# Kernel tuning notes

Measured on AMD Instinct MI355X. Metric: run time of the kernel, lower is better.

The kernel has to match this reference:

```python
import jax, jax.numpy as jnp
import numpy as np

ACT_BIT = 8
W_BIT = 8
EPS = 1e-8


def ste_round(x):
    # straight-through round (matches torch STE quant autograd)
    return x + jax.lax.stop_gradient(jnp.round(x) - x)


def quant_act(x):
    """Per-tensor symmetric 8-bit activation quantization (HAWQ QuantAct)."""
    n = 2 ** (ACT_BIT - 1) - 1  # 127
    x_max = jax.lax.stop_gradient(jnp.max(jnp.abs(x)))
    scale = jnp.maximum(x_max, EPS) / n
    x_int = jnp.clip(ste_round(x / scale), -n - 1, n)
    return x_int * scale, scale


def quant_linear(x_q, act_scale, weight, bias):
    """Per-channel symmetric 8-bit weight quant + integer matmul + fused dequant."""
    n = 2 ** (W_BIT - 1) - 1  # 127
    w_max = jax.lax.stop_gradient(jnp.max(jnp.abs(weight), axis=1, keepdims=True))  # [out,1]
    w_scale = jnp.maximum(w_max, EPS) / n                                            # [out,1]
    w_int = jnp.clip(ste_round(weight / w_scale), -n - 1, n)                         # [out,in]
    bias_scale = w_scale[:, 0] * act_scale                                           # [out]
    b_int = ste_round(bias / bias_scale)                                             # [out]
    x_int = x_q / act_scale                                   # integer-valued float, [..., in]
    out_int = jnp.einsum('...i,oi->...o', x_int, w_int)       # int8-domain GEMM in float
    return (out_int + b_int) * bias_scale                     # fused dequant


def setup_inputs() -> dict:
    key = jax.random.key(0)
    k1, k2, k3 = jax.random.split(key, 3)
    L, B, Q, D, O = 6, 8, 1024, 1024, 1024
    hs = jax.random.normal(k1, (L, B, Q, D), dtype=jnp.float32)
    weight = jax.random.normal(k2, (O, D), dtype=jnp.float32) * 0.02
    bias = jax.random.normal(k3, (O,), dtype=jnp.float32) * 0.02
    return {"hs": hs, "weight": weight, "bias": bias}


def reference(hs, weight, bias):
    x_q, act_scale = quant_act(hs)
    return quant_linear(x_q, act_scale, weight, bias)
```

## Files before the change

### kernel.cpp

```cpp
#include <hip/hip_runtime.h>
#include <stdint.h>

typedef int i32x4 __attribute__((ext_vector_type(4)));

#define K_DIM 1024
#define BM 256
#define BN 256
#define BKK 64
#define NKT (K_DIM / BKK)


__device__ __forceinline__ int quant1(float v, float inv) {
  float t = rintf(v * inv);
  t = fminf(fmaxf(t, -128.0f), 127.0f);
  return (int)t;
}

__device__ __forceinline__ void gld_lds16(const signed char* g, signed char* l) {
  typedef const __attribute__((address_space(1))) unsigned int* gp_t;
  typedef __attribute__((address_space(3))) unsigned int* lp_t;
  __builtin_amdgcn_global_load_lds((gp_t)(const void*)g, (lp_t)(void*)l, 16, 0, 0);
}

#define SB __builtin_amdgcn_sched_barrier(0)
#define BAR __builtin_amdgcn_s_barrier()
#define WAIT_LGKM0 asm volatile("s_waitcnt lgkmcnt(0)" ::: "memory")

__global__ void absmax_part(const float* __restrict__ x, float* __restrict__ parts,
                            long long n4) {
  long long i = (long long)blockIdx.x * blockDim.x + threadIdx.x;
  const long long stride = (long long)gridDim.x * blockDim.x;
  const float4* x4 = (const float4*)x;
  float m = 0.0f;
  for (; i < n4; i += stride) {
    float4 v = x4[i];
    m = fmaxf(m, fmaxf(fmaxf(fabsf(v.x), fabsf(v.y)), fmaxf(fabsf(v.z), fabsf(v.w))));
  }
#pragma unroll
  for (int off = 32; off > 0; off >>= 1) m = fmaxf(m, __shfl_down(m, off, 64));
  __shared__ float sm[4];
  const int lane = threadIdx.x & 63, wid = threadIdx.x >> 6;
  if (lane == 0) sm[wid] = m;
  __syncthreads();
  if (threadIdx.x == 0)
    parts[blockIdx.x] = fmaxf(fmaxf(sm[0], sm[1]), fmaxf(sm[2], sm[3]));
}

__global__ void absmax_fin(const float* __restrict__ parts, unsigned int* __restrict__ amax_u,
                           int nparts) {
  const int t = threadIdx.x;
  float m = 0.0f;
  for (int i = t; i < nparts; i += 256) m = fmaxf(m, parts[i]);
#pragma unroll
  for (int off = 32; off > 0; off >>= 1) m = fmaxf(m, __shfl_down(m, off, 64));
  __shared__ float sm[4];
  const int lane = t & 63, wid = t >> 6;
  if (lane == 0) sm[wid] = m;
  __syncthreads();
  if (t == 0)
    amax_u[0] = __float_as_uint(fmaxf(fmaxf(sm[0], sm[1]), fmaxf(sm[2], sm[3])));
}

__global__ void wquant_kernel(const float* __restrict__ w, const float* __restrict__ bias,
                              const unsigned int* __restrict__ amax_u,
                              signed char* __restrict__ wq,
                              float* __restrict__ bscale, float* __restrict__ bint) {
  const int o = blockIdx.x;
  const int t = threadIdx.x;
  float4 v = ((const float4*)(w + (size_t)o * K_DIM))[t];
  float m = fmaxf(fmaxf(fabsf(v.x), fabsf(v.y)), fmaxf(fabsf(v.z), fabsf(v.w)));
#pragma unroll
  for (int off = 32; off > 0; off >>= 1) m = fmaxf(m, __shfl_down(m, off, 64));
  __shared__ float sm[4];
  __shared__ float s_scale;
  const int lane = t & 63, wid = t >> 6;
  if (lane == 0) sm[wid] = m;
  __syncthreads();
  if (t == 0) {
    float wm = fmaxf(fmaxf(sm[0], sm[1]), fmaxf(sm[2], sm[3]));
    float wsc = fmaxf(wm, 1e-8f) / 127.0f;
    float asc = fmaxf(__uint_as_float(*amax_u), 1e-8f) / 127.0f;
    float bsc = wsc * asc;
    bscale[o] = bsc;
    bint[o] = rintf(bias[o] / bsc);
    s_scale = wsc;
  }
  __syncthreads();
  const float inv = 1.0f / s_scale;
  int q0 = quant1(v.x, inv), q1 = quant1(v.y, inv), q2 = quant1(v.z, inv), q3 = quant1(v.w, inv);
  unsigned int p = (unsigned)(q0 & 255) | ((unsigned)(q1 & 255) << 8) |
                   ((unsigned)(q2 & 255) << 16) | ((unsigned)(q3 & 255) << 24);
  const int F = o >> 4, T = t >> 4;
  const int l = (((t >> 2) & 3) << 4) | (o & 15);
  const int j = (t << 2) & 15;
  *(unsigned int*)(wq + (((size_t)F << 14) + (T << 10) + (l << 4) + j)) = p;
}

__global__ void aquant_kernel(const float* __restrict__ x, const unsigned int* __restrict__ amax_u,
                              uint4* __restrict__ q16, int nchunk) {
  const float asc = fmaxf(__uint_as_float(*amax_u), 1e-8f) / 127.0f;
  const float inv = 1.0f / asc;
  int c = blockIdx.x * blockDim.x + threadIdx.x;
  const int stride = gridDim.x * blockDim.x;
  for (; c < nchunk; c += stride) {
    const int l = c & 63, T = (c >> 6) & 15, F = c >> 10;
    const size_t src = (((size_t)(F << 4) + (l & 15)) << 10) + (T << 6) + ((l >> 4) << 4);
    const float4* s4 = (const float4*)(x + src);
    unsigned int r[4];
#pragma unroll
    for (int q = 0; q < 4; q++) {
      float4 v = s4[q];
      int q0 = quant1(v.x, inv), q1 = quant1(v.y, inv), q2 = quant1(v.z, inv), q3 = quant1(v.w, inv);
      r[q] = (unsigned)(q0 & 255) | ((unsigned)(q1 & 255) << 8) |
             ((unsigned)(q2 & 255) << 16) | ((unsigned)(q3 & 255) << 24);
    }
    q16[c] = make_uint4(r[0], r[1], r[2], r[3]);
  }
}

__global__ __launch_bounds__(512, 2) void gemm_kernel(
    const signed char* __restrict__ A, const signed char* __restrict__ W,
    const float* __restrict__ bscale, const float* __restrict__ bint,
    float* __restrict__ out, int M, int N, int K) {
  extern __shared__ __align__(16) signed char smem[];
  signed char* Abase = smem;

  const int nwg = gridDim.x;
  const int orig = blockIdx.x;
  const int wgid = (orig & 7) * (nwg >> 3) + (orig >> 3);
  const int nbn = N / BN;
  const int bm = wgid / nbn;
  const int bn = wgid % nbn;
  const int m0 = bm * BM, n0 = bn * BN;

  const int tid = threadIdx.x;
  const int lane = tid & 63;
  const int wid = tid >> 6;
  const int wr = wid >> 1 >> 1;
  const int wc = wid & 3;

  const signed char* gaf = A + (((size_t)(m0 >> 4) + wid) << 14) + (lane << 4);
  const size_t fs8 = (size_t)8 << 14;
  const signed char* gbf = W + (((size_t)(n0 >> 4) + wc * 4) << 14) + (lane << 4);

  i32x4 acc[8][4];
#pragma unroll
  for (int i = 0; i < 8; i++)
#pragma unroll
    for (int j = 0; j < 4; j++) acc[i][j] = (i32x4){0, 0, 0, 0};

  i32x4 af[8];
  i32x4 bfA[4], bfB[4];

#define LOADB(L, tt)                                                           \
  do {                                                                         \
    L[0] = *(const i32x4*)(gbf + ((size_t)0 << 14) + ((tt) << 10));            \
    L[1] = *(const i32x4*)(gbf + ((size_t)1 << 14) + ((tt) << 10));            \
    L[2] = *(const i32x4*)(gbf + ((size_t)2 << 14) + ((tt) << 10));            \
    L[3] = *(const i32x4*)(gbf + ((size_t)3 << 14) + ((tt) << 10));            \
  } while (0)

#define ISSUEA(tt)                                                             \
  do {                                                                         \
    gld_lds16(gaf + ((size_t)(tt) << 10),                                      \
              Abase + ((((tt) & 3) * 16 + wid) << 10));                        \
    gld_lds16(gaf + fs8 + ((size_t)(tt) << 10),                                \
              Abase + ((((tt) & 3) * 16 + wid + 8) << 10));                    \
  } while (0)

#define RD_A(t, i_)                                                            \
  af[i_] = *(const i32x4*)(Abase + ((((t) & 3) * 16 + wr * 8 + (i_)) << 10) + (lane << 4))

#define MFMA16U(IB, U)                                                         \
  do {                                                                         \
    __builtin_amdgcn_s_setprio(1);                                             \
    _Pragma("unroll") for (int i_ = 0; i_ < 4; i_++)                           \
      _Pragma("unroll") for (int j_ = 0; j_ < 4; j_++)                         \
        acc[(IB) + i_][j_] = __builtin_amdgcn_mfma_i32_16x16x64_i8(            \
            af[(IB) + i_], U[j_], acc[(IB) + i_][j_], 0, 0, 0);                \
    __builtin_amdgcn_s_setprio(0);                                             \
  } while (0)

#define TILE(t, U, L, DOB, DOA, VMW, DOVM)                                     \
  do {                                                                         \
    if (DOB) LOADB(L, (t) + 1);                                                \
    if (DOA) ISSUEA((t) + 3);                                                  \
    SB;                                                                        \
    RD_A(t, 0); RD_A(t, 1); RD_A(t, 2); RD_A(t, 3);                            \
    RD_A(t, 4); RD_A(t, 5); RD_A(t, 6); RD_A(t, 7);                            \
    MFMA16U(0, U);                                                             \
    MFMA16U(4, U);                                                             \
    if (DOVM) { asm volatile("s_waitcnt " VMW ::: "memory"); }                 \
    SB; BAR; SB;                                                               \
  } while (0)

  ISSUEA(0); ISSUEA(1); ISSUEA(2);
  LOADB(bfA, 0);
  asm volatile("s_waitcnt vmcnt(0)" ::: "memory");
  SB; BAR; SB;

  TILE(0,  bfA, bfB, 1, 1, "vmcnt(8)", 1);
  TILE(1,  bfB, bfA, 1, 1, "vmcnt(8)", 1);
  TILE(2,  bfA, bfB, 1, 1, "vmcnt(8)", 1);
  TILE(3,  bfB, bfA, 1, 1, "vmcnt(8)", 1);
  TILE(4,  bfA, bfB, 1, 1, "vmcnt(8)", 1);
  TILE(5,  bfB, bfA, 1, 1, "vmcnt(8)", 1);
  TILE(6,  bfA, bfB, 1, 1, "vmcnt(8)", 1);
  TILE(7,  bfB, bfA, 1, 1, "vmcnt(8)", 1);
  TILE(8,  bfA, bfB, 1, 1, "vmcnt(8)", 1);
  TILE(9,  bfB, bfA, 1, 1, "vmcnt(8)", 1);
  TILE(10, bfA, bfB, 1, 1, "vmcnt(8)", 1);
  TILE(11, bfB, bfA, 1, 1, "vmcnt(8)", 1);
  TILE(12, bfA, bfB, 1, 1, "vmcnt(8)", 1);
  TILE(13, bfB, bfA, 1, 0, "vmcnt(6)", 1);
  TILE(14, bfA, bfB, 1, 0, "vmcnt(4)", 1);
  TILE(15, bfB, bfA, 0, 0, "", 0);

#undef TILE
#undef MFMA16U
#undef RD_A
#undef ISSUEA
#undef LOADB

  float* Cst = (float*)smem;
  const int rr = (lane >> 4) * 4;
  const int cc = lane & 15;
#pragma unroll
  for (int q = 0; q < 4; ++q) {
    if (wr == (q >> 1)) {
#pragma unroll
      for (int j = 0; j < 4; j++) {
        const int colL = wc * 64 + j * 16 + cc;
        const float bs = bscale[n0 + colL];
        const float bi = bint[n0 + colL];
#pragma unroll
        for (int i2 = 0; i2 < 4; i2++) {
          const int i = (q & 1) * 4 + i2;
#pragma unroll
          for (int r = 0; r < 4; r++)
            Cst[(i2 * 16 + rr + r) * 256 + colL] = ((float)acc[i][j][r] + bi) * bs;
        }
      }
    }
    WAIT_LGKM0;
    BAR;
    const size_t rowbase = (size_t)(m0 + q * 64) * N + n0;
#pragma unroll
    for (int it = 0; it < 8; ++it) {
      const int r_ = it * 8 + wid;
      float4 v = *(const float4*)&Cst[r_ * 256 + lane * 4];
      *(float4*)&out[rowbase + (size_t)r_ * N + lane * 4] = v;
    }
    WAIT_LGKM0;
    BAR;
  }
}

extern "C" void kernel_launch(void* const* d_in, const int* in_sizes, int n_in,
                              void* d_out, int out_size, void* d_ws, size_t ws_size,
                              hipStream_t stream) {
  const float* hs = (const float*)d_in[0];
  const float* w = (const float*)d_in[1];
  const float* bias = (const float*)d_in[2];
  float* out = (float*)d_out;

  const long long n = (long long)in_sizes[0];
  const int K = K_DIM;
  const int O = in_sizes[2];
  const int M = (int)(n / K);

  char* ws = (char*)d_ws;
  unsigned int* amax_u = (unsigned int*)ws;
  float* parts = (float*)(ws + 1024);
  float* bscale = (float*)(ws + 16384);
  float* bint = (float*)(ws + 20480);
  signed char* wq = (signed char*)(ws + 65536);
  signed char* xq = (signed char*)(ws + 65536 + 1048576);

  hipFuncSetAttribute((const void*)gemm_kernel,
                      hipFuncAttributeMaxDynamicSharedMemorySize, 65536);

  const long long n4 = n / 4;
  absmax_part<<<2048, 256, 0, stream>>>(hs, parts, n4);
  absmax_fin<<<1, 256, 0, stream>>>(parts, amax_u, 2048);
  wquant_kernel<<<O, 256, 0, stream>>>(w, bias, amax_u, wq, bscale, bint);
  const int nchunk = (int)(n / 16);
  aquant_kernel<<<2048, 256, 0, stream>>>(hs, amax_u, (uint4*)xq, nchunk);

  const int nblocks = (M / BM) * (O / BN);
  gemm_kernel<<<nblocks, 512, 65536, stream>>>(xq, wq, bscale, bint, out, M, O, K);
}
```

Baseline: 180.2 us.

## Shrink GEMM tiles to 128x128 with 4 waves and stage activation quant via LDS

The GEMM tile drops from 256x256 with 8 waves to 128x128 with 4 waves. That halves the LDS footprint to 32 KB and raises the intended occupancy to 3 blocks per CU, and it gives 4x more workgroups for better CU balance. The activation-quant kernel now gives one block per 16-row fragment: it reads rows coalesced, transposes into the MFMA fragment layout in shared memory, then writes contiguous uint4s, which replaces the old scattered strided gather. The initial wait is relaxed from vmcnt(0) to vmcnt(8). Smaller tiles lower operand reuse and raise global/L2 traffic for A and W.

```diff
diff --git a/kernel.cpp b/kernel.cpp
--- a/kernel.cpp
+++ b/kernel.cpp
@@ -4,8 +4,8 @@
 typedef int i32x4 __attribute__((ext_vector_type(4)));
 
 #define K_DIM 1024
-#define BM 256
-#define BN 256
+#define BM 128
+#define BN 128
 #define BKK 64
 #define NKT (K_DIM / BKK)
 
@@ -96,29 +96,37 @@
   *(unsigned int*)(wq + (((size_t)F << 14) + (T << 10) + (l << 4) + j)) = p;
 }
 
-__global__ void aquant_kernel(const float* __restrict__ x, const unsigned int* __restrict__ amax_u,
-                              uint4* __restrict__ q16, int nchunk) {
+__global__ __launch_bounds__(256) void aquant_kernel(
+    const float* __restrict__ x, const unsigned int* __restrict__ amax_u,
+    uint4* __restrict__ q16) {
+  __shared__ unsigned int limg[4096];
   const float asc = fmaxf(__uint_as_float(*amax_u), 1e-8f) / 127.0f;
   const float inv = 1.0f / asc;
-  int c = blockIdx.x * blockDim.x + threadIdx.x;
-  const int stride = gridDim.x * blockDim.x;
-  for (; c < nchunk; c += stride) {
-    const int l = c & 63, T = (c >> 6) & 15, F = c >> 10;
-    const size_t src = (((size_t)(F << 4) + (l & 15)) << 10) + (T << 6) + ((l >> 4) << 4);
-    const float4* s4 = (const float4*)(x + src);
-    unsigned int r[4];
-#pragma unroll
-    for (int q = 0; q < 4; q++) {
-      float4 v = s4[q];
-      int q0 = quant1(v.x, inv), q1 = quant1(v.y, inv), q2 = quant1(v.z, inv), q3 = quant1(v.w, inv);
-      r[q] = (unsigned)(q0 & 255) | ((unsigned)(q1 & 255) << 8) |
-             ((unsigned)(q2 & 255) << 16) | ((unsigned)(q3 & 255) << 24);
-    }
-    q16[c] = make_uint4(r[0], r[1], r[2], r[3]);
-  }
-}
-
-__global__ __launch_bounds__(512, 2) void gemm_kernel(
+  const int F = blockIdx.x;
+  const int t = threadIdx.x;
+  const int r = t >> 4, kq = t & 15;
+  const float* rowp = x + (((size_t)F * 16 + r) << 10);
+#pragma unroll
+  for (int rep = 0; rep < 16; ++rep) {
+    const int fi = rep * 16 + kq;
+    float4 v = ((const float4*)rowp)[fi];
+    int q0 = quant1(v.x, inv), q1 = quant1(v.y, inv), q2 = quant1(v.z, inv), q3 = quant1(v.w, inv);
+    unsigned int p = (unsigned)(q0 & 255) | ((unsigned)(q1 & 255) << 8) |
+                     ((unsigned)(q2 & 255) << 16) | ((unsigned)(q3 & 255) << 24);
+    const int k0 = fi << 2;
+    const int T = k0 >> 6;
+    const int l = (((k0 >> 4) & 3) << 4) | r;
+    const int j = k0 & 15;
+    limg[(T << 8) + (l << 2) + (j >> 2)] = p;
+  }
+  __syncthreads();
+  const uint4* src = (const uint4*)limg;
+#pragma unroll
+  for (int rep2 = 0; rep2 < 4; ++rep2)
+    q16[((size_t)F << 10) + rep2 * 256 + t] = src[rep2 * 256 + t];
+}
+
+__global__ __launch_bounds__(256, 3) void gemm_kernel(
     const signed char* __restrict__ A, const signed char* __restrict__ W,
     const float* __restrict__ bscale, const float* __restrict__ bint,
     float* __restrict__ out, int M, int N, int K) {
@@ -136,20 +144,20 @@
   const int tid = threadIdx.x;
   const int lane = tid & 63;
   const int wid = tid >> 6;
-  const int wr = wid >> 1 >> 1;
-  const int wc = wid & 3;
+  const int wr = wid >> 1;
+  const int wc = wid & 1;
 
   const signed char* gaf = A + (((size_t)(m0 >> 4) + wid) << 14) + (lane << 4);
-  const size_t fs8 = (size_t)8 << 14;
+  const size_t fs4 = (size_t)4 << 14;
   const signed char* gbf = W + (((size_t)(n0 >> 4) + wc * 4) << 14) + (lane << 4);
 
-  i32x4 acc[8][4];
-#pragma unroll
-  for (int i = 0; i < 8; i++)
+  i32x4 acc[4][4];
+#pragma unroll
+  for (int i = 0; i < 4; i++)
 #pragma unroll
     for (int j = 0; j < 4; j++) acc[i][j] = (i32x4){0, 0, 0, 0};
 
-  i32x4 af[8];
+  i32x4 af[4];
   i32x4 bfA[4], bfB[4];
 
 #define LOADB(L, tt)                                                           \
@@ -163,21 +171,21 @@
 #define ISSUEA(tt)                                                             \
   do {                                                                         \
     gld_lds16(gaf + ((size_t)(tt) << 10),                                      \
-              Abase + ((((tt) & 3) * 16 + wid) << 10));                        \
-    gld_lds16(gaf + fs8 + ((size_t)(tt) << 10),                                \
-              Abase + ((((tt) & 3) * 16 + wid + 8) << 10));                    \
+              Abase + ((((tt) & 3) * 8 + wid) << 10));                         \
+    gld_lds16(gaf + fs4 + ((size_t)(tt) << 10),                                \
+              Abase + ((((tt) & 3) * 8 + wid + 4) << 10));                     \
   } while (0)
 
 #define RD_A(t, i_)                                                            \
-  af[i_] = *(const i32x4*)(Abase + ((((t) & 3) * 16 + wr * 8 + (i_)) << 10) + (lane << 4))
-
-#define MFMA16U(IB, U)                                                         \
+  af[i_] = *(const i32x4*)(Abase + ((((t) & 3) * 8 + wr * 4 + (i_)) << 10) + (lane << 4))
+
+#define MFMA16U(U)                                                             \
   do {                                                                         \
     __builtin_amdgcn_s_setprio(1);                                             \
     _Pragma("unroll") for (int i_ = 0; i_ < 4; i_++)                           \
       _Pragma("unroll") for (int j_ = 0; j_ < 4; j_++)                         \
-        acc[(IB) + i_][j_] = __builtin_amdgcn_mfma_i32_16x16x64_i8(            \
-            af[(IB) + i_], U[j_], acc[(IB) + i_][j_], 0, 0, 0);                \
+        acc[i_][j_] = __builtin_amdgcn_mfma_i32_16x16x64_i8(                   \
+            af[i_], U[j_], acc[i_][j_], 0, 0, 0);                              \
     __builtin_amdgcn_s_setprio(0);                                             \
   } while (0)
 
@@ -187,16 +195,14 @@
     if (DOA) ISSUEA((t) + 3);                                                  \
     SB;                                                                        \
     RD_A(t, 0); RD_A(t, 1); RD_A(t, 2); RD_A(t, 3);                            \
-    RD_A(t, 4); RD_A(t, 5); RD_A(t, 6); RD_A(t, 7);                            \
-    MFMA16U(0, U);                                                             \
-    MFMA16U(4, U);                                                             \
+    MFMA16U(U);                                                                \
     if (DOVM) { asm volatile("s_waitcnt " VMW ::: "memory"); }                 \
     SB; BAR; SB;                                                               \
   } while (0)
 
   ISSUEA(0); ISSUEA(1); ISSUEA(2);
   LOADB(bfA, 0);
-  asm volatile("s_waitcnt vmcnt(0)" ::: "memory");
+  asm volatile("s_waitcnt vmcnt(8)" ::: "memory");
   SB; BAR; SB;
 
   TILE(0,  bfA, bfB, 1, 1, "vmcnt(8)", 1);
@@ -226,30 +232,29 @@
   const int rr = (lane >> 4) * 4;
   const int cc = lane & 15;
 #pragma unroll
-  for (int q = 0; q < 4; ++q) {
-    if (wr == (q >> 1)) {
+  for (int h = 0; h < 2; ++h) {
+    if (wr == h) {
 #pragma unroll
       for (int j = 0; j < 4; j++) {
         const int colL = wc * 64 + j * 16 + cc;
         const float bs = bscale[n0 + colL];
         const float bi = bint[n0 + colL];
 #pragma unroll
-        for (int i2 = 0; i2 < 4; i2++) {
-          const int i = (q & 1) * 4 + i2;
+        for (int i = 0; i < 4; i++)
 #pragma unroll
           for (int r = 0; r < 4; r++)
-            Cst[(i2 * 16 + rr + r) * 256 + colL] = ((float)acc[i][j][r] + bi) * bs;
-        }
+            Cst[(i * 16 + rr + r) * 128 + colL] = ((float)acc[i][j][r] + bi) * bs;
       }
     }
     WAIT_LGKM0;
     BAR;
-    const size_t rowbase = (size_t)(m0 + q * 64) * N + n0;
+    const size_t rowbase = (size_t)(m0 + h * 64) * N + n0;
 #pragma unroll
     for (int it = 0; it < 8; ++it) {
-      const int r_ = it * 8 + wid;
-      float4 v = *(const float4*)&Cst[r_ * 256 + lane * 4];
-      *(float4*)&out[rowbase + (size_t)r_ * N + lane * 4] = v;
+      const int r_ = it * 8 + wid * 2 + (lane >> 5);
+      const int c_ = (lane & 31) * 4;
+      float4 v = *(const float4*)&Cst[r_ * 128 + c_];
+      *(float4*)&out[rowbase + (size_t)r_ * N + c_] = v;
     }
     WAIT_LGKM0;
     BAR;
@@ -277,16 +282,12 @@
   signed char* wq = (signed char*)(ws + 65536);
   signed char* xq = (signed char*)(ws + 65536 + 1048576);
 
-  hipFuncSetAttribute((const void*)gemm_kernel,
-                      hipFuncAttributeMaxDynamicSharedMemorySize, 65536);
-
   const long long n4 = n / 4;
   absmax_part<<<2048, 256, 0, stream>>>(hs, parts, n4);
   absmax_fin<<<1, 256, 0, stream>>>(parts, amax_u, 2048);
   wquant_kernel<<<O, 256, 0, stream>>>(w, bias, amax_u, wq, bscale, bint);
-  const int nchunk = (int)(n / 16);
-  aquant_kernel<<<2048, 256, 0, stream>>>(hs, amax_u, (uint4*)xq, nchunk);
+  aquant_kernel<<<M / 16, 256, 0, stream>>>(hs, amax_u, (uint4*)xq);
 
   const int nblocks = (M / BM) * (O / BN);
-  gemm_kernel<<<nblocks, 512, 65536, stream>>>(xq, wq, bscale, bint, out, M, O, K);
-}
+  gemm_kernel<<<nblocks, 256, 32768, stream>>>(xq, wq, bscale, bint, out, M, O, K);
+}
```

Result: slower. 189.2 us (+5.0%).

## Fold absmax finalize into quant kernels and stage activation packing in LDS

Applied to the files above, without the earlier changes.

Drops the single-block absmax finalize launch. Each wquant and aquant block now re-reduces the 2048 partial maxima itself. The activation quant kernel now runs one block per 16-row fragment. Each thread reads contiguous row segments, writes the packed int8 into an LDS image in the MFMA layout, then stores it out as coalesced uint4 writes. This replaces the old strided gather reads. The cost is a redundant 8KB parts read per block and a much larger grid of 3072 blocks with 16KB of LDS each.

```diff
diff --git a/kernel.cpp b/kernel.cpp
--- a/kernel.cpp
+++ b/kernel.cpp
@@ -6,8 +6,7 @@
 #define K_DIM 1024
 #define BM 256
 #define BN 256
-#define BKK 64
-#define NKT (K_DIM / BKK)
+#define NKT 16
 
 
 __device__ __forceinline__ int quant1(float v, float inv) {
@@ -25,6 +24,19 @@
 #define SB __builtin_amdgcn_sched_barrier(0)
 #define BAR __builtin_amdgcn_s_barrier()
 #define WAIT_LGKM0 asm volatile("s_waitcnt lgkmcnt(0)" ::: "memory")
+
+__device__ __forceinline__ float reduce_parts(const float* __restrict__ parts,
+                                              float* sm ) {
+  const int t = threadIdx.x;
+  float m = 0.0f;
+  for (int i = t; i < 2048; i += 256) m = fmaxf(m, parts[i]);
+#pragma unroll
+  for (int off = 32; off > 0; off >>= 1) m = fmaxf(m, __shfl_down(m, off, 64));
+  const int lane = t & 63, wid = t >> 6;
+  if (lane == 0) sm[wid] = m;
+  __syncthreads();
+  return fmaxf(fmaxf(sm[0], sm[1]), fmaxf(sm[2], sm[3]));
+}
 
 __global__ void absmax_part(const float* __restrict__ x, float* __restrict__ parts,
                             long long n4) {
@@ -46,25 +58,12 @@
     parts[blockIdx.x] = fmaxf(fmaxf(sm[0], sm[1]), fmaxf(sm[2], sm[3]));
 }
 
-__global__ void absmax_fin(const float* __restrict__ parts, unsigned int* __restrict__ amax_u,
-                           int nparts) {
-  const int t = threadIdx.x;
-  float m = 0.0f;
-  for (int i = t; i < nparts; i += 256) m = fmaxf(m, parts[i]);
-#pragma unroll
-  for (int off = 32; off > 0; off >>= 1) m = fmaxf(m, __shfl_down(m, off, 64));
-  __shared__ float sm[4];
-  const int lane = t & 63, wid = t >> 6;
-  if (lane == 0) sm[wid] = m;
-  __syncthreads();
-  if (t == 0)
-    amax_u[0] = __float_as_uint(fmaxf(fmaxf(sm[0], sm[1]), fmaxf(sm[2], sm[3])));
-}
-
 __global__ void wquant_kernel(const float* __restrict__ w, const float* __restrict__ bias,
-                              const unsigned int* __restrict__ amax_u,
+                              const float* __restrict__ parts,
                               signed char* __restrict__ wq,
                               float* __restrict__ bscale, float* __restrict__ bint) {
+  __shared__ float smr[4];
+  const float amax = reduce_parts(parts, smr);
   const int o = blockIdx.x;
   const int t = threadIdx.x;
   float4 v = ((const float4*)(w + (size_t)o * K_DIM))[t];
@@ -79,7 +78,7 @@
   if (t == 0) {
     float wm = fmaxf(fmaxf(sm[0], sm[1]), fmaxf(sm[2], sm[3]));
     float wsc = fmaxf(wm, 1e-8f) / 127.0f;
-    float asc = fmaxf(__uint_as_float(*amax_u), 1e-8f) / 127.0f;
+    float asc = fmaxf(amax, 1e-8f) / 127.0f;
     float bsc = wsc * asc;
     bscale[o] = bsc;
     bint[o] = rintf(bias[o] / bsc);
@@ -96,26 +95,36 @@
   *(unsigned int*)(wq + (((size_t)F << 14) + (T << 10) + (l << 4) + j)) = p;
 }
 
-__global__ void aquant_kernel(const float* __restrict__ x, const unsigned int* __restrict__ amax_u,
-                              uint4* __restrict__ q16, int nchunk) {
-  const float asc = fmaxf(__uint_as_float(*amax_u), 1e-8f) / 127.0f;
+__global__ __launch_bounds__(256) void aquant_kernel(
+    const float* __restrict__ x, const float* __restrict__ parts,
+    uint4* __restrict__ q16) {
+  __shared__ float smr[4];
+  __shared__ unsigned int limg[4096];
+  const float amax = reduce_parts(parts, smr);
+  const float asc = fmaxf(amax, 1e-8f) / 127.0f;
   const float inv = 1.0f / asc;
-  int c = blockIdx.x * blockDim.x + threadIdx.x;
-  const int stride = gridDim.x * blockDim.x;
-  for (; c < nchunk; c += stride) {
-    const int l = c & 63, T = (c >> 6) & 15, F = c >> 10;
-    const size_t src = (((size_t)(F << 4) + (l & 15)) << 10) + (T << 6) + ((l >> 4) << 4);
-    const float4* s4 = (const float4*)(x + src);
-    unsigned int r[4];
-#pragma unroll
-    for (int q = 0; q < 4; q++) {
-      float4 v = s4[q];
-      int q0 = quant1(v.x, inv), q1 = quant1(v.y, inv), q2 = quant1(v.z, inv), q3 = quant1(v.w, inv);
-      r[q] = (unsigned)(q0 & 255) | ((unsigned)(q1 & 255) << 8) |
-             ((unsigned)(q2 & 255) << 16) | ((unsigned)(q3 & 255) << 24);
-    }
-    q16[c] = make_uint4(r[0], r[1], r[2], r[3]);
-  }
+  const int F = blockIdx.x;
+  const int t = threadIdx.x;
+  const int r = t >> 4, kq = t & 15;
+  const float* rowp = x + (((size_t)F * 16 + r) << 10);
+#pragma unroll
+  for (int rep = 0; rep < 16; ++rep) {
+    const int fi = rep * 16 + kq;
+    float4 v = ((const float4*)rowp)[fi];
+    int q0 = quant1(v.x, inv), q1 = quant1(v.y, inv), q2 = quant1(v.z, inv), q3 = quant1(v.w, inv);
+    unsigned int p = (unsigned)(q0 & 255) | ((unsigned)(q1 & 255) << 8) |
+                     ((unsigned)(q2 & 255) << 16) | ((unsigned)(q3 & 255) << 24);
+    const int k0 = fi << 2;
+    const int T = k0 >> 6;
+    const int l = (((k0 >> 4) & 3) << 4) | r;
+    const int j = k0 & 15;
+    limg[(T << 8) + (l << 2) + (j >> 2)] = p;
+  }
+  __syncthreads();
+  const uint4* src = (const uint4*)limg;
+#pragma unroll
+  for (int rep2 = 0; rep2 < 4; ++rep2)
+    q16[((size_t)F << 10) + rep2 * 256 + t] = src[rep2 * 256 + t];
 }
 
 __global__ __launch_bounds__(512, 2) void gemm_kernel(
@@ -136,7 +145,7 @@
   const int tid = threadIdx.x;
   const int lane = tid & 63;
   const int wid = tid >> 6;
-  const int wr = wid >> 1 >> 1;
+  const int wr = wid >> 2;
   const int wc = wid & 3;
 
   const signed char* gaf = A + (((size_t)(m0 >> 4) + wid) << 14) + (lane << 4);
@@ -270,7 +279,6 @@
   const int M = (int)(n / K);
 
   char* ws = (char*)d_ws;
-  unsigned int* amax_u = (unsigned int*)ws;
   float* parts = (float*)(ws + 1024);
   float* bscale = (float*)(ws + 16384);
   float* bint = (float*)(ws + 20480);
@@ -282,10 +290,8 @@
 
   const long long n4 = n / 4;
   absmax_part<<<2048, 256, 0, stream>>>(hs, parts, n4);
-  absmax_fin<<<1, 256, 0, stream>>>(parts, amax_u, 2048);
-  wquant_kernel<<<O, 256, 0, stream>>>(w, bias, amax_u, wq, bscale, bint);
-  const int nchunk = (int)(n / 16);
-  aquant_kernel<<<2048, 256, 0, stream>>>(hs, amax_u, (uint4*)xq, nchunk);
+  wquant_kernel<<<O, 256, 0, stream>>>(w, bias, parts, wq, bscale, bint);
+  aquant_kernel<<<M / 16, 256, 0, stream>>>(hs, parts, (uint4*)xq);
 
   const int nblocks = (M / BM) * (O / BN);
   gemm_kernel<<<nblocks, 512, 65536, stream>>>(xq, wq, bscale, bint, out, M, O, K);
```

After: 190.4 us. 1.06x slower.

## Halve GEMM N-tile to 128 with 4x2 wave grid and higher occupancy

Applied to the files above, without the earlier changes.

The output tile shrinks from 256x256 to 256x128 and the 8 waves are rearranged as 4 rows by 2 columns, so each wave holds half as many accumulators and A fragments. Launch bounds are raised to target 4 workgroups per CU, and the epilogue staging is reworked for the narrower tile. The aim is more concurrent workgroups and lower register pressure to hide latency. In exchange each A tile is reused across fewer columns, which doubles A traffic per output and halves MFMA work per barrier.

```diff
diff --git a/kernel.cpp b/kernel.cpp
--- a/kernel.cpp
+++ b/kernel.cpp
@@ -5,9 +5,8 @@
 
 #define K_DIM 1024
 #define BM 256
-#define BN 256
-#define BKK 64
-#define NKT (K_DIM / BKK)
+#define BN 128
+#define NKT 16
 
 
 __device__ __forceinline__ int quant1(float v, float inv) {
@@ -118,7 +117,7 @@
   }
 }
 
-__global__ __launch_bounds__(512, 2) void gemm_kernel(
+__global__ __launch_bounds__(512, 4) void gemm_kernel(
     const signed char* __restrict__ A, const signed char* __restrict__ W,
     const float* __restrict__ bscale, const float* __restrict__ bint,
     float* __restrict__ out, int M, int N, int K) {
@@ -136,20 +135,20 @@
   const int tid = threadIdx.x;
   const int lane = tid & 63;
   const int wid = tid >> 6;
-  const int wr = wid >> 1 >> 1;
-  const int wc = wid & 3;
+  const int wr = wid >> 1;
+  const int wc = wid & 1;
 
   const signed char* gaf = A + (((size_t)(m0 >> 4) + wid) << 14) + (lane << 4);
   const size_t fs8 = (size_t)8 << 14;
   const signed char* gbf = W + (((size_t)(n0 >> 4) + wc * 4) << 14) + (lane << 4);
 
-  i32x4 acc[8][4];
-#pragma unroll
-  for (int i = 0; i < 8; i++)
+  i32x4 acc[4][4];
+#pragma unroll
+  for (int i = 0; i < 4; i++)
 #pragma unroll
     for (int j = 0; j < 4; j++) acc[i][j] = (i32x4){0, 0, 0, 0};
 
-  i32x4 af[8];
+  i32x4 af[4];
   i32x4 bfA[4], bfB[4];
 
 #define LOADB(L, tt)                                                           \
@@ -169,15 +168,15 @@
   } while (0)
 
 #define RD_A(t, i_)                                                            \
-  af[i_] = *(const i32x4*)(Abase + ((((t) & 3) * 16 + wr * 8 + (i_)) << 10) + (lane << 4))
-
-#define MFMA16U(IB, U)                                                         \
+  af[i_] = *(const i32x4*)(Abase + ((((t) & 3) * 16 + wr * 4 + (i_)) << 10) + (lane << 4))
+
+#define MFMA16U(U)                                                             \
   do {                                                                         \
     __builtin_amdgcn_s_setprio(1);                                             \
     _Pragma("unroll") for (int i_ = 0; i_ < 4; i_++)                           \
       _Pragma("unroll") for (int j_ = 0; j_ < 4; j_++)                         \
-        acc[(IB) + i_][j_] = __builtin_amdgcn_mfma_i32_16x16x64_i8(            \
-            af[(IB) + i_], U[j_], acc[(IB) + i_][j_], 0, 0, 0);                \
+        acc[i_][j_] = __builtin_amdgcn_mfma_i32_16x16x64_i8(                   \
+            af[i_], U[j_], acc[i_][j_], 0, 0, 0);                              \
     __builtin_amdgcn_s_setprio(0);                                             \
   } while (0)
 
@@ -187,9 +186,7 @@
     if (DOA) ISSUEA((t) + 3);                                                  \
     SB;                                                                        \
     RD_A(t, 0); RD_A(t, 1); RD_A(t, 2); RD_A(t, 3);                            \
-    RD_A(t, 4); RD_A(t, 5); RD_A(t, 6); RD_A(t, 7);                            \
-    MFMA16U(0, U);                                                             \
-    MFMA16U(4, U);                                                             \
+    MFMA16U(U);                                                                \
     if (DOVM) { asm volatile("s_waitcnt " VMW ::: "memory"); }                 \
     SB; BAR; SB;                                                               \
   } while (0)
@@ -227,29 +224,28 @@
   const int cc = lane & 15;
 #pragma unroll
   for (int q = 0; q < 4; ++q) {
-    if (wr == (q >> 1)) {
+    if (wr == q) {
 #pragma unroll
       for (int j = 0; j < 4; j++) {
         const int colL = wc * 64 + j * 16 + cc;
         const float bs = bscale[n0 + colL];
         const float bi = bint[n0 + colL];
 #pragma unroll
-        for (int i2 = 0; i2 < 4; i2++) {
-          const int i = (q & 1) * 4 + i2;
+        for (int i = 0; i < 4; i++)
 #pragma unroll
           for (int r = 0; r < 4; r++)
-            Cst[(i2 * 16 + rr + r) * 256 + colL] = ((float)acc[i][j][r] + bi) * bs;
-        }
+            Cst[(i * 16 + rr + r) * 128 + colL] = ((float)acc[i][j][r] + bi) * bs;
       }
     }
     WAIT_LGKM0;
     BAR;
     const size_t rowbase = (size_t)(m0 + q * 64) * N + n0;
 #pragma unroll
-    for (int it = 0; it < 8; ++it) {
-      const int r_ = it * 8 + wid;
-      float4 v = *(const float4*)&Cst[r_ * 256 + lane * 4];
-      *(float4*)&out[rowbase + (size_t)r_ * N + lane * 4] = v;
+    for (int it = 0; it < 4; ++it) {
+      const int r_ = it * 16 + wid * 2 + (lane >> 5);
+      const int c_ = (lane & 31) * 4;
+      float4 v = *(const float4*)&Cst[r_ * 128 + c_];
+      *(float4*)&out[rowbase + (size_t)r_ * N + c_] = v;
     }
     WAIT_LGKM0;
     BAR;
```

New measurement: 214.9 us. +19.2%, slower.
